# Kernel tuning notes

Hardware: AMD Instinct MI355X
Metric: run time of the kernel (lower is better)

Reference implementation:

```python
import jax, jax.numpy as jnp
import numpy as np

NUM_GROUPS = 32
EPS = 1e-6


def group_norm(x, w, b):
    # x: (B, C, L); normalize per group of C//32 channels over (channels-in-group, L)
    B, C, L = x.shape
    xg = x.reshape(B, NUM_GROUPS, C // NUM_GROUPS, L)
    mean = jnp.mean(xg, axis=(2, 3), keepdims=True)
    var = jnp.var(xg, axis=(2, 3), keepdims=True)
    xn = ((xg - mean) * jax.lax.rsqrt(var + EPS)).reshape(B, C, L)
    return xn * w[None, :, None] + b[None, :, None]


def conv1x1(x, w, b):
    # 1x1 Conv1d == channel-mixing linear. x: (B,C,L), w: (O,C), b: (O,)
    return jnp.einsum('oc,bcl->bol', w, x) + b[None, :, None]


def setup_inputs() -> dict:
    key = jax.random.key(0)
    ks = jax.random.split(key, 6)
    B, C, L = 8, 512, 2048
    s = 1.0 / np.sqrt(C)
    return {
        'x': jax.random.normal(ks[0], (B, C, L), dtype=jnp.float32),
        'gn_w': jnp.ones((C,), jnp.float32),
        'gn_b': jnp.zeros((C,), jnp.float32),
        'wq': jax.random.normal(ks[1], (C, C), dtype=jnp.float32) * s,
        'bq': jnp.zeros((C,), jnp.float32),
        'wk': jax.random.normal(ks[2], (C, C), dtype=jnp.float32) * s,
        'bk': jnp.zeros((C,), jnp.float32),
        'wv': jax.random.normal(ks[3], (C, C), dtype=jnp.float32) * s,
        'bv': jnp.zeros((C,), jnp.float32),
        'wo': jax.random.normal(ks[4], (C, C), dtype=jnp.float32) * s,
        'bo': jnp.zeros((C,), jnp.float32),
    }


def reference(x, gn_w, gn_b, wq, bq, wk, bk, wv, bv, wo, bo):
    B, C, L = x.shape
    h = group_norm(x, gn_w, gn_b)
    q = conv1x1(h, wq, bq)  # (B,C,L)
    k = conv1x1(h, wk, bk)
    v = conv1x1(h, wv, bv)
    scale = jnp.asarray(C, x.dtype) ** -0.5
    # scores over length: w[b,i,j] = sum_c q[b,c,i] k[b,c,j]
    w_ = jnp.einsum('bci,bcj->bij', q, k) * scale
    w_ = jax.nn.softmax(w_, axis=-1)
    # h[b,c,i] = sum_j w[b,i,j] v[b,c,j]
    h = jnp.einsum('bij,bcj->bci', w_, v)
    h = conv1x1(h, wo, bo)
    return x + h
```

## Files before the change

kernel.cpp:

```cpp
#include <hip/hip_runtime.h>
#include <math.h>

#define BATCH 8
#define CH 512
#define LEN 2048
#define NG 32
#define CPG 16

typedef unsigned short u16;
typedef __bf16 bf16x8 __attribute__((ext_vector_type(8)));
typedef float f32x16 __attribute__((ext_vector_type(16)));

__device__ __forceinline__ u16 f2bf(float f) {
    union { float f; unsigned u; } c; c.f = f;
    unsigned r = c.u + 0x7fffu + ((c.u >> 16) & 1u);
    return (u16)(r >> 16);
}
__device__ __forceinline__ float bf2f(u16 h) {
    union { unsigned u; float f; } c; c.u = ((unsigned)h) << 16;
    return c.f;
}
__device__ __forceinline__ void gload16(const u16* g, u16* l) {
    __builtin_amdgcn_global_load_lds(
        (const __attribute__((address_space(1))) unsigned int*)g,
        (__attribute__((address_space(3))) unsigned int*)l, 16, 0, 0);
}

#define BARRIER() do {                                   \
    asm volatile("" ::: "memory");                       \
    __builtin_amdgcn_s_barrier();                        \
    asm volatile("" ::: "memory");                       \
} while (0)

__global__ __launch_bounds__(256) void zerof4(float4* __restrict__ p) {
    p[blockIdx.x * 256 + threadIdx.x] = make_float4(0.f, 0.f, 0.f, 0.f);
}

__global__ __launch_bounds__(256) void wconv4(const float* __restrict__ w0, const float* __restrict__ w1,
                                              const float* __restrict__ w2, const float* __restrict__ w3,
                                              u16* __restrict__ o0, u16* __restrict__ o1,
                                              u16* __restrict__ o2, u16* __restrict__ o3) {
    const float* s; u16* d;
    switch (blockIdx.y) {
        case 0: s = w0; d = o0; break;
        case 1: s = w1; d = o1; break;
        case 2: s = w2; d = o2; break;
        default: s = w3; d = o3; break;
    }
    const int i = blockIdx.x * 256 + threadIdx.x;
    float4 f = ((const float4*)s)[i];
    ushort4 o = make_ushort4(f2bf(f.x), f2bf(f.y), f2bf(f.z), f2bf(f.w));
    ((ushort4*)d)[i] = o;
}

__global__ __launch_bounds__(256) void gn_stats(const float* __restrict__ x,
                                                const float* __restrict__ gw,
                                                const float* __restrict__ gb,
                                                float* __restrict__ gnA,
                                                float* __restrict__ gnB) {
    const int b = blockIdx.x >> 5, g = blockIdx.x & 31;
    const float4* xp = (const float4*)(x + ((size_t)b * CH + (size_t)g * CPG) * LEN);
    float s = 0.f, s2 = 0.f;
    for (int i = threadIdx.x; i < (CPG * LEN) / 4; i += 256) {
        float4 v = xp[i];
        s += v.x + v.y + v.z + v.w;
        s2 = fmaf(v.x, v.x, fmaf(v.y, v.y, fmaf(v.z, v.z, fmaf(v.w, v.w, s2))));
    }
    #pragma unroll
    for (int off = 32; off > 0; off >>= 1) {
        s  += __shfl_down(s, off, 64);
        s2 += __shfl_down(s2, off, 64);
    }
    __shared__ float sm[2][4];
    const int lane = threadIdx.x & 63, wv = threadIdx.x >> 6;
    if (lane == 0) { sm[0][wv] = s; sm[1][wv] = s2; }
    __syncthreads();
    if (threadIdx.x < CPG) {
        const float S  = sm[0][0] + sm[0][1] + sm[0][2] + sm[0][3];
        const float S2 = sm[1][0] + sm[1][1] + sm[1][2] + sm[1][3];
        const float mean = S * (1.f / (CPG * LEN));
        const float var  = S2 * (1.f / (CPG * LEN)) - mean * mean;
        const float rstd = rsqrtf(var + 1e-6f);
        const int c = g * CPG + threadIdx.x;
        const float sc = rstd * gw[c];
        gnA[b * CH + c] = sc;
        gnB[b * CH + c] = gb[c] - mean * sc;
    }
}

__global__ __launch_bounds__(256) void gn_apply_t(const float* __restrict__ x,
                                                  const float* __restrict__ gnA,
                                                  const float* __restrict__ gnB,
                                                  u16* __restrict__ Ht) {
    __shared__ float tile[64][65];
    const int b = blockIdx.z, c0 = blockIdx.y * 64, l0 = blockIdx.x * 64;
    const int t = threadIdx.x, tl = t & 63, tr = t >> 6;
    #pragma unroll 4
    for (int i = 0; i < 16; ++i) {
        const int c = tr + i * 4;
        const float a = gnA[b * CH + c0 + c];
        const float sh = gnB[b * CH + c0 + c];
        tile[c][tl] = x[((size_t)b * CH + c0 + c) * LEN + l0 + tl] * a + sh;
    }
    __syncthreads();
    #pragma unroll 4
    for (int i = 0; i < 16; ++i) {
        const int l = tr + i * 4;
        Ht[((size_t)b * LEN + l0 + l) * CH + c0 + tl] = f2bf(tile[tl][l]);
    }
}

#define EPI_QK   0
#define EPI_TBN  1
#define EPI_EXP  2
#define EPI_TNRM 3
#define EPI_FIN  4

template <int MODE, int BM>
__global__ __launch_bounds__(512, 2) void gemm256(
    const u16* __restrict__ A, int lda, long long sA,
    const u16* __restrict__ B, int ldb, long long sB,
    void* __restrict__ Out, void* __restrict__ Out2,
    int ldo, long long sO,
    const float* __restrict__ bias, const float* __restrict__ bias2,
    const float* __restrict__ res, long long sR,
    float* __restrict__ rsum, long long sRS,
    int K, float alpha) {
    constexpr int MF = BM / 64;
    constexpr int RA = BM / 64;
    __shared__ u16 As[2][BM * 64];
    __shared__ u16 Bs[2][256 * 64];

    const int gx = gridDim.x, gy = gridDim.y;
    int flat = (blockIdx.z * gy + blockIdx.y) * gx + blockIdx.x;
    const int nb = gx * gy * (int)gridDim.z;
    flat = (flat & 7) * (nb >> 3) + (flat >> 3);
    const int bz = flat / (gx * gy);
    const int rr = flat - bz * gx * gy;
    const int by = rr / gx;
    const int bx = rr - by * gx;

    const int n0 = bx * 256, m0 = by * BM;
    A += (size_t)bz * sA;
    B += (size_t)bz * sB;

    const int t = threadIdx.x;
    const int lane = t & 63, wid = t >> 6;
    const int col = lane & 31, half = lane >> 5;
    const int wm = (wid >> 2) * (BM / 2), wn = (wid & 3) * 64;

    const int rowL = t >> 3;
    const int kq = ((t & 7) ^ (rowL & 7)) * 8;
    const u16* gA[RA];
    const u16* gB[4];
    #pragma unroll
    for (int r = 0; r < RA; ++r) gA[r] = A + (size_t)(m0 + r * 64 + rowL) * lda + kq;
    #pragma unroll
    for (int r = 0; r < 4; ++r)  gB[r] = B + (size_t)(n0 + r * 64 + rowL) * ldb + kq;
    const int dst = t * 8;

    f32x16 acc[MF][2];
    #pragma unroll
    for (int mi = 0; mi < MF; ++mi)
        #pragma unroll
        for (int nj = 0; nj < 2; ++nj)
            acc[mi][nj] = (f32x16)(0.f);

    #pragma unroll
    for (int r = 0; r < RA; ++r) { gload16(gA[r], &As[0][r * 4096 + dst]); gA[r] += 64; }
    #pragma unroll
    for (int r = 0; r < 4; ++r)  { gload16(gB[r], &Bs[0][r * 4096 + dst]); gB[r] += 64; }
    asm volatile("s_waitcnt vmcnt(0)" ::: "memory");
    BARRIER();

    const int NT = K >> 6;
    const int cw8 = col & 7;

    for (int kt = 0; kt < NT; ++kt) {
        const int cur = kt & 1;
        const u16* __restrict__ Ab = As[cur];
        const u16* __restrict__ Bb = Bs[cur];
        u16* Ad = As[cur ^ 1];
        u16* Bd = Bs[cur ^ 1];
        const bool pf = (kt + 1 < NT);

        #pragma unroll
        for (int p = 0; p < 2; ++p) {
            const int s0 = ((4 * p + half) ^ cw8) * 8;
            const int s1 = ((4 * p + 2 + half) ^ cw8) * 8;
            bf16x8 av[MF][2], bv[2][2];
            #pragma unroll
            for (int mi = 0; mi < MF; ++mi) {
                const u16* base = Ab + (wm + mi * 32 + col) * 64;
                av[mi][0] = *(const bf16x8*)(base + s0);
                av[mi][1] = *(const bf16x8*)(base + s1);
            }
            #pragma unroll
            for (int nj = 0; nj < 2; ++nj) {
                const u16* base = Bb + (wn + nj * 32 + col) * 64;
                bv[nj][0] = *(const bf16x8*)(base + s0);
                bv[nj][1] = *(const bf16x8*)(base + s1);
            }
            if (pf) {
                if (p == 0) {
                    #pragma unroll
                    for (int r = 0; r < RA / 2; ++r) { gload16(gA[r], Ad + r * 4096 + dst); gA[r] += 64; }
                    #pragma unroll
                    for (int r = 0; r < 2; ++r)      { gload16(gB[r], Bd + r * 4096 + dst); gB[r] += 64; }
                } else {
                    #pragma unroll
                    for (int r = RA / 2; r < RA; ++r) { gload16(gA[r], Ad + r * 4096 + dst); gA[r] += 64; }
                    #pragma unroll
                    for (int r = 2; r < 4; ++r)       { gload16(gB[r], Bd + r * 4096 + dst); gB[r] += 64; }
                }
            }
            BARRIER();
            __builtin_amdgcn_s_setprio(1);
            #pragma unroll
            for (int h = 0; h < 2; ++h)
                #pragma unroll
                for (int mi = 0; mi < MF; ++mi)
                    #pragma unroll
                    for (int nj = 0; nj < 2; ++nj)
                        acc[mi][nj] = __builtin_amdgcn_mfma_f32_32x32x16_bf16(
                            av[mi][h], bv[nj][h], acc[mi][nj], 0, 0, 0);
            __builtin_amdgcn_s_setprio(0);
            if (p == 0) BARRIER();
        }
        asm volatile("s_waitcnt vmcnt(0)" ::: "memory");
        BARRIER();
    }

    if (MODE == EPI_FIN) {
        float* O = (float*)Out + (size_t)bz * sO;
        const float* R = res + (size_t)bz * sR;
        #pragma unroll
        for (int im = 0; im < MF; ++im)
            #pragma unroll
            for (int g4 = 0; g4 < 4; ++g4) {
                const int mb = m0 + wm + im * 32 + g4 * 8 + half * 4;
                #pragma unroll
                for (int jn = 0; jn < 2; ++jn) {
                    const int n = n0 + wn + jn * 32 + col;
                    const float bb = bias[n];
                    const size_t base = (size_t)n * ldo + mb;
                    const float4 r4 = *(const float4*)&R[base];
                    float4 o4;
                    o4.x = acc[im][jn][g4 * 4 + 0] + bb + r4.x;
                    o4.y = acc[im][jn][g4 * 4 + 1] + bb + r4.y;
                    o4.z = acc[im][jn][g4 * 4 + 2] + bb + r4.z;
                    o4.w = acc[im][jn][g4 * 4 + 3] + bb + r4.w;
                    *(float4*)&O[base] = o4;
                }
            }
    } else if (MODE == EPI_EXP) {
        u16* O = (u16*)Out + (size_t)bz * sO;
        float* RS = rsum + (size_t)bz * sRS;
        float psum[2] = {0.f, 0.f};
        #pragma unroll
        for (int im = 0; im < MF; ++im)
            #pragma unroll
            for (int g4 = 0; g4 < 4; ++g4) {
                const int mb = m0 + wm + im * 32 + g4 * 8 + half * 4;
                #pragma unroll
                for (int jn = 0; jn < 2; ++jn) {
                    const int n = n0 + wn + jn * 32 + col;
                    u16 h0 = f2bf(__expf(acc[im][jn][g4 * 4 + 0] * alpha));
                    u16 h1 = f2bf(__expf(acc[im][jn][g4 * 4 + 1] * alpha));
                    u16 h2 = f2bf(__expf(acc[im][jn][g4 * 4 + 2] * alpha));
                    u16 h3 = f2bf(__expf(acc[im][jn][g4 * 4 + 3] * alpha));
                    psum[jn] += bf2f(h0) + bf2f(h1) + bf2f(h2) + bf2f(h3);
                    *(ushort4*)&O[(size_t)n * ldo + mb] = make_ushort4(h0, h1, h2, h3);
                }
            }
        #pragma unroll
        for (int jn = 0; jn < 2; ++jn) psum[jn] += __shfl_xor(psum[jn], 32, 64);
        if (half == 0) {
            #pragma unroll
            for (int jn = 0; jn < 2; ++jn)
                atomicAdd(&RS[n0 + wn + jn * 32 + col], psum[jn]);
        }
    } else {
        u16* O;
        const float* bi = bias;
        const float* RS = (MODE == EPI_TNRM) ? rsum + (size_t)bz * sRS : nullptr;
        int mbase = m0 + wm;
        if (MODE == EPI_QK) {
            const bool hi = (m0 & 512) != 0;
            O  = (u16*)(hi ? Out2 : Out) + (size_t)bz * sO;
            bi = hi ? bias2 : bias;
            mbase = (m0 & 511) + wm;
        } else {
            O = (u16*)Out + (size_t)bz * sO;
        }
        float inv[2];
        if (MODE == EPI_TNRM) {
            inv[0] = 1.f / RS[n0 + wn + col];
            inv[1] = 1.f / RS[n0 + wn + 32 + col];
        }
        #pragma unroll
        for (int im = 0; im < MF; ++im)
            #pragma unroll
            for (int g4 = 0; g4 < 4; ++g4) {
                const int mb = mbase + im * 32 + g4 * 8 + half * 4;
                float4 bm = make_float4(0.f, 0.f, 0.f, 0.f);
                if (MODE == EPI_QK) bm = *(const float4*)&bi[mb];
                #pragma unroll
                for (int jn = 0; jn < 2; ++jn) {
                    const int n = n0 + wn + jn * 32 + col;
                    float v0 = acc[im][jn][g4 * 4 + 0];
                    float v1 = acc[im][jn][g4 * 4 + 1];
                    float v2 = acc[im][jn][g4 * 4 + 2];
                    float v3 = acc[im][jn][g4 * 4 + 3];
                    if (MODE == EPI_QK)  { v0 += bm.x; v1 += bm.y; v2 += bm.z; v3 += bm.w; }
                    if (MODE == EPI_TBN) { const float bb = bi[n]; v0 += bb; v1 += bb; v2 += bb; v3 += bb; }
                    if (MODE == EPI_TNRM) { v0 *= inv[jn]; v1 *= inv[jn]; v2 *= inv[jn]; v3 *= inv[jn]; }
                    ushort4 pk = make_ushort4(f2bf(v0), f2bf(v1), f2bf(v2), f2bf(v3));
                    *(ushort4*)&O[(size_t)n * ldo + mb] = pk;
                }
            }
    }
}

extern "C" void kernel_launch(void* const* d_in, const int* in_sizes, int n_in,
                              void* d_out, int out_size, void* d_ws, size_t ws_size,
                              hipStream_t stream) {
    const float* x    = (const float*)d_in[0];
    const float* gn_w = (const float*)d_in[1];
    const float* gn_b = (const float*)d_in[2];
    const float* wq   = (const float*)d_in[3];
    const float* bq   = (const float*)d_in[4];
    const float* wk   = (const float*)d_in[5];
    const float* bk   = (const float*)d_in[6];
    const float* wv   = (const float*)d_in[7];
    const float* bv   = (const float*)d_in[8];
    const float* wo   = (const float*)d_in[9];
    const float* bo   = (const float*)d_in[10];
    float* out = (float*)d_out;

    char* p = (char*)d_ws;
    const size_t WSZ = (size_t)CH * CH * 2;
    const size_t HSZ = (size_t)BATCH * CH * LEN * 2;
    u16* Wqk = (u16*)p; p += 2 * WSZ;
    u16* Wvb = (u16*)p; p += WSZ;
    u16* Wob = (u16*)p; p += WSZ;
    u16* Ht  = (u16*)p; p += HSZ;
    u16* Qt  = (u16*)p; p += HSZ;
    u16* Kt  = (u16*)p; p += HSZ;
    u16* Vb  = (u16*)p; p += HSZ;
    u16* Sb  = (u16*)p; p += (size_t)BATCH * LEN * LEN * 2;
    float* gnA = (float*)p; p += (size_t)BATCH * CH * 4;
    float* gnB = (float*)p; p += (size_t)BATCH * CH * 4;
    float* rowsum = (float*)p;

    const long long sH = (long long)LEN * CH;
    const long long sV = (long long)CH * LEN;
    const long long sS = (long long)LEN * LEN;
    const float scale = 0.04419417382415922f;

    wconv4<<<dim3(256, 4), 256, 0, stream>>>(wq, wk, wv, wo,
                                             Wqk, Wqk + (size_t)CH * CH, Wvb, Wob);
    gn_stats<<<BATCH * NG, 256, 0, stream>>>(x, gn_w, gn_b, gnA, gnB);
    gn_apply_t<<<dim3(LEN / 64, CH / 64, BATCH), 256, 0, stream>>>(x, gnA, gnB, Ht);
    zerof4<<<BATCH * LEN / 1024, 256, 0, stream>>>((float4*)rowsum);

    gemm256<EPI_QK, 256><<<dim3(8, 4, 8), 512, 0, stream>>>(
        Wqk, CH, 0, Ht, CH, sH, Qt, Kt, CH, sH, bq, bk, nullptr, 0, nullptr, 0, CH, 0.f);
    gemm256<EPI_TBN, 128><<<dim3(2, 16, 8), 512, 0, stream>>>(
        Ht, CH, sH, Wvb, CH, 0, Vb, nullptr, LEN, sV, bv, nullptr, nullptr, 0, nullptr, 0, CH, 0.f);
    gemm256<EPI_EXP, 256><<<dim3(8, 8, 8), 512, 0, stream>>>(
        Kt, CH, sH, Qt, CH, sH, Sb, nullptr, LEN, sS, nullptr, nullptr, nullptr, 0, rowsum, LEN, CH, scale);
    gemm256<EPI_TNRM, 128><<<dim3(8, 4, 8), 512, 0, stream>>>(
        Vb, LEN, sV, Sb, LEN, sS, Ht, nullptr, CH, sH, nullptr, nullptr, nullptr, 0, rowsum, LEN, LEN, 0.f);
    gemm256<EPI_FIN, 128><<<dim3(2, 16, 8), 512, 0, stream>>>(
        Ht, CH, sH, Wob, CH, 0, out, nullptr, LEN, sV, bo, nullptr, x, sV, nullptr, 0, CH, 0.f);
}
```

Before: 301.5 us.

## Switch GEMMs to triple-buffered 256x128 tiles with two-stage-ahead prefetch

Replaces the double-buffered GEMM template with a fixed 256x128 tile kernel that keeps three LDS stages and prefetches two K-tiles ahead, using partial vmcnt waits so loads overlap more compute. Warp layout changes to a 4x2 grid of 64x64 subtiles, and all five GEMM launches are re-gridded for the new tile shape. The deeper pipeline is meant to hide global-load latency. In exchange it uses more LDS per block, which may limit occupancy, and it halves the N tile for the stages that used 256-wide tiles.

```diff
diff --git a/kernel.cpp b/kernel.cpp
--- a/kernel.cpp
+++ b/kernel.cpp
@@ -116,8 +116,8 @@
 #define EPI_TNRM 3
 #define EPI_FIN  4
 
-template <int MODE, int BM>
-__global__ __launch_bounds__(512, 2) void gemm256(
+template <int MODE>
+__global__ __launch_bounds__(512, 2) void gemm_p3(
     const u16* __restrict__ A, int lda, long long sA,
     const u16* __restrict__ B, int ldb, long long sB,
     void* __restrict__ Out, void* __restrict__ Out2,
@@ -126,71 +126,65 @@
     const float* __restrict__ res, long long sR,
     float* __restrict__ rsum, long long sRS,
     int K, float alpha) {
-    constexpr int MF = BM / 64;
-    constexpr int RA = BM / 64;
-    __shared__ u16 As[2][BM * 64];
-    __shared__ u16 Bs[2][256 * 64];
+    __shared__ u16 As[3][256 * 64];
+    __shared__ u16 Bs[3][128 * 64];
 
     const int gx = gridDim.x, gy = gridDim.y;
     int flat = (blockIdx.z * gy + blockIdx.y) * gx + blockIdx.x;
-    const int nb = gx * gy * (int)gridDim.z;
-    flat = (flat & 7) * (nb >> 3) + (flat >> 3);
+    const int nbk = gx * gy * (int)gridDim.z;
+    flat = (flat & 7) * (nbk >> 3) + (flat >> 3);
     const int bz = flat / (gx * gy);
-    const int rr = flat - bz * gx * gy;
-    const int by = rr / gx;
-    const int bx = rr - by * gx;
-
-    const int n0 = bx * 256, m0 = by * BM;
+    const int r2 = flat - bz * gx * gy;
+    const int by = r2 / gx;
+    const int bx = r2 - by * gx;
+
+    const int n0 = bx * 128, m0 = by * 256;
     A += (size_t)bz * sA;
     B += (size_t)bz * sB;
 
     const int t = threadIdx.x;
     const int lane = t & 63, wid = t >> 6;
     const int col = lane & 31, half = lane >> 5;
-    const int wm = (wid >> 2) * (BM / 2), wn = (wid & 3) * 64;
+    const int wm = (wid >> 1) * 64, wn = (wid & 1) * 64;
+    const int cw8 = col & 7;
 
     const int rowL = t >> 3;
     const int kq = ((t & 7) ^ (rowL & 7)) * 8;
-    const u16* gA[RA];
-    const u16* gB[4];
+    const u16* gA[4];
+    const u16* gB[2];
     #pragma unroll
-    for (int r = 0; r < RA; ++r) gA[r] = A + (size_t)(m0 + r * 64 + rowL) * lda + kq;
+    for (int r = 0; r < 4; ++r) gA[r] = A + (size_t)(m0 + r * 64 + rowL) * lda + kq;
     #pragma unroll
-    for (int r = 0; r < 4; ++r)  gB[r] = B + (size_t)(n0 + r * 64 + rowL) * ldb + kq;
+    for (int r = 0; r < 2; ++r) gB[r] = B + (size_t)(n0 + r * 64 + rowL) * ldb + kq;
     const int dst = t * 8;
 
-    f32x16 acc[MF][2];
+    f32x16 acc[2][2];
     #pragma unroll
-    for (int mi = 0; mi < MF; ++mi)
+    for (int mi = 0; mi < 2; ++mi)
         #pragma unroll
         for (int nj = 0; nj < 2; ++nj)
             acc[mi][nj] = (f32x16)(0.f);
 
-    #pragma unroll
-    for (int r = 0; r < RA; ++r) { gload16(gA[r], &As[0][r * 4096 + dst]); gA[r] += 64; }
-    #pragma unroll
-    for (int r = 0; r < 4; ++r)  { gload16(gB[r], &Bs[0][r * 4096 + dst]); gB[r] += 64; }
-    asm volatile("s_waitcnt vmcnt(0)" ::: "memory");
-    BARRIER();
-
-    const int NT = K >> 6;
-    const int cw8 = col & 7;
-
-    for (int kt = 0; kt < NT; ++kt) {
-        const int cur = kt & 1;
-        const u16* __restrict__ Ab = As[cur];
-        const u16* __restrict__ Bb = Bs[cur];
-        u16* Ad = As[cur ^ 1];
-        u16* Bd = Bs[cur ^ 1];
-        const bool pf = (kt + 1 < NT);
-
+    auto stage = [&](u16* Ad, u16* Bd, int part) {
+        if (part == 0) {
+            gload16(gA[0], Ad + 0 * 4096 + dst); gA[0] += 64;
+            gload16(gA[1], Ad + 1 * 4096 + dst); gA[1] += 64;
+            gload16(gA[2], Ad + 2 * 4096 + dst); gA[2] += 64;
+        } else {
+            gload16(gA[3], Ad + 3 * 4096 + dst); gA[3] += 64;
+            gload16(gB[0], Bd + 0 * 4096 + dst); gB[0] += 64;
+            gload16(gB[1], Bd + 1 * 4096 + dst); gB[1] += 64;
+        }
+    };
+
+    auto tile = [&](const u16* Ab, const u16* Bb, u16* Af, u16* Bf, bool pf) {
         #pragma unroll
         for (int p = 0; p < 2; ++p) {
             const int s0 = ((4 * p + half) ^ cw8) * 8;
             const int s1 = ((4 * p + 2 + half) ^ cw8) * 8;
-            bf16x8 av[MF][2], bv[2][2];
-            #pragma unroll
-            for (int mi = 0; mi < MF; ++mi) {
+            bf16x8 av[2][2], bv[2][2];
+            #pragma unroll
+            for (int mi = 0; mi < 2; ++mi) {
                 const u16* base = Ab + (wm + mi * 32 + col) * 64;
                 av[mi][0] = *(const bf16x8*)(base + s0);
                 av[mi][1] = *(const bf16x8*)(base + s1);
@@ -201,25 +195,13 @@
                 bv[nj][0] = *(const bf16x8*)(base + s0);
                 bv[nj][1] = *(const bf16x8*)(base + s1);
             }
-            if (pf) {
-                if (p == 0) {
-                    #pragma unroll
-                    for (int r = 0; r < RA / 2; ++r) { gload16(gA[r], Ad + r * 4096 + dst); gA[r] += 64; }
-                    #pragma unroll
-                    for (int r = 0; r < 2; ++r)      { gload16(gB[r], Bd + r * 4096 + dst); gB[r] += 64; }
-                } else {
-                    #pragma unroll
-                    for (int r = RA / 2; r < RA; ++r) { gload16(gA[r], Ad + r * 4096 + dst); gA[r] += 64; }
-                    #pragma unroll
-                    for (int r = 2; r < 4; ++r)       { gload16(gB[r], Bd + r * 4096 + dst); gB[r] += 64; }
-                }
-            }
+            if (pf) stage(Af, Bf, p);
             BARRIER();
             __builtin_amdgcn_s_setprio(1);
             #pragma unroll
             for (int h = 0; h < 2; ++h)
                 #pragma unroll
-                for (int mi = 0; mi < MF; ++mi)
+                for (int mi = 0; mi < 2; ++mi)
                     #pragma unroll
                     for (int nj = 0; nj < 2; ++nj)
                         acc[mi][nj] = __builtin_amdgcn_mfma_f32_32x32x16_bf16(
@@ -227,15 +209,34 @@
             __builtin_amdgcn_s_setprio(0);
             if (p == 0) BARRIER();
         }
-        asm volatile("s_waitcnt vmcnt(0)" ::: "memory");
+    };
+
+    u16 *A0 = As[0], *A1 = As[1], *A2 = As[2];
+    u16 *B0 = Bs[0], *B1 = Bs[1], *B2 = Bs[2];
+
+    stage(A0, B0, 0); stage(A0, B0, 1);
+    stage(A1, B1, 0); stage(A1, B1, 1);
+    asm volatile("s_waitcnt vmcnt(6)" ::: "memory");
+    BARRIER();
+
+    const int NT = K >> 6;
+    for (int kt = 0; kt < NT - 2; ++kt) {
+        tile(A0, B0, A2, B2, true);
+        asm volatile("s_waitcnt vmcnt(6)" ::: "memory");
         BARRIER();
-    }
+        u16* tA = A0; A0 = A1; A1 = A2; A2 = tA;
+        u16* tB = B0; B0 = B1; B1 = B2; B2 = tB;
+    }
+    tile(A0, B0, nullptr, nullptr, false);
+    asm volatile("s_waitcnt vmcnt(0)" ::: "memory");
+    BARRIER();
+    tile(A1, B1, nullptr, nullptr, false);
 
     if (MODE == EPI_FIN) {
         float* O = (float*)Out + (size_t)bz * sO;
         const float* R = res + (size_t)bz * sR;
         #pragma unroll
-        for (int im = 0; im < MF; ++im)
+        for (int im = 0; im < 2; ++im)
             #pragma unroll
             for (int g4 = 0; g4 < 4; ++g4) {
                 const int mb = m0 + wm + im * 32 + g4 * 8 + half * 4;
@@ -258,7 +259,7 @@
         float* RS = rsum + (size_t)bz * sRS;
         float psum[2] = {0.f, 0.f};
         #pragma unroll
-        for (int im = 0; im < MF; ++im)
+        for (int im = 0; im < 2; ++im)
             #pragma unroll
             for (int g4 = 0; g4 < 4; ++g4) {
                 const int mb = m0 + wm + im * 32 + g4 * 8 + half * 4;
@@ -299,7 +300,7 @@
             inv[1] = 1.f / RS[n0 + wn + 32 + col];
         }
         #pragma unroll
-        for (int im = 0; im < MF; ++im)
+        for (int im = 0; im < 2; ++im)
             #pragma unroll
             for (int g4 = 0; g4 < 4; ++g4) {
                 const int mb = mbase + im * 32 + g4 * 8 + half * 4;
@@ -364,14 +365,14 @@
     gn_apply_t<<<dim3(LEN / 64, CH / 64, BATCH), 256, 0, stream>>>(x, gnA, gnB, Ht);
     zerof4<<<BATCH * LEN / 1024, 256, 0, stream>>>((float4*)rowsum);
 
-    gemm256<EPI_QK, 256><<<dim3(8, 4, 8), 512, 0, stream>>>(
+    gemm_p3<EPI_QK><<<dim3(16, 4, 8), 512, 0, stream>>>(
         Wqk, CH, 0, Ht, CH, sH, Qt, Kt, CH, sH, bq, bk, nullptr, 0, nullptr, 0, CH, 0.f);
-    gemm256<EPI_TBN, 128><<<dim3(2, 16, 8), 512, 0, stream>>>(
+    gemm_p3<EPI_TBN><<<dim3(4, 8, 8), 512, 0, stream>>>(
         Ht, CH, sH, Wvb, CH, 0, Vb, nullptr, LEN, sV, bv, nullptr, nullptr, 0, nullptr, 0, CH, 0.f);
-    gemm256<EPI_EXP, 256><<<dim3(8, 8, 8), 512, 0, stream>>>(
+    gemm_p3<EPI_EXP><<<dim3(16, 8, 8), 512, 0, stream>>>(
         Kt, CH, sH, Qt, CH, sH, Sb, nullptr, LEN, sS, nullptr, nullptr, nullptr, 0, rowsum, LEN, CH, scale);
-    gemm256<EPI_TNRM, 128><<<dim3(8, 4, 8), 512, 0, stream>>>(
+    gemm_p3<EPI_TNRM><<<dim3(16, 2, 8), 512, 0, stream>>>(
         Vb, LEN, sV, Sb, LEN, sS, Ht, nullptr, CH, sH, nullptr, nullptr, nullptr, 0, rowsum, LEN, LEN, 0.f);
-    gemm256<EPI_FIN, 128><<<dim3(2, 16, 8), 512, 0, stream>>>(
+    gemm_p3<EPI_FIN><<<dim3(4, 8, 8), 512, 0, stream>>>(
         Ht, CH, sH, Wob, CH, 0, out, nullptr, LEN, sV, bo, nullptr, x, sV, nullptr, 0, CH, 0.f);
 }
```

New measurement: 299.7 us. No clear change (-0.6%).
